# Kernel tuning notes

Measured on AMD Instinct MI355X. Metric: run time of the kernel, lower is better.

## Reference

```python
import jax, jax.numpy as jnp
import numpy as np

N = 50000   # nodes (subjects in population graph)
E = 800000  # edges (similarity graph, avg degree 16)
F = 128     # node features


def setup_inputs() -> dict:
    key = jax.random.key(0)
    ks = jax.random.split(key, 8)

    def glorot(k, shape):
        scale = 1.0 / np.sqrt(shape[0])
        return jax.random.normal(k, shape, jnp.float32) * scale

    x = jax.random.normal(ks[0], (N, F), jnp.float32)
    edge_index = jax.random.randint(ks[1], (2, E), 0, N, dtype=jnp.int64)
    return {
        "x": x,
        "edge_index": edge_index,
        "W1": glorot(ks[2], (F, 128)),   "b1": jnp.zeros((128,), jnp.float32),
        "W2": glorot(ks[3], (128, 64)),  "b2": jnp.zeros((64,), jnp.float32),
        "Wf1": glorot(ks[4], (64, 32)),  "bf1": jnp.zeros((32,), jnp.float32),
        "Wf2": glorot(ks[5], (32, 1)),   "bf2": jnp.zeros((1,), jnp.float32),
    }


def reference(x, edge_index, W1, b1, W2, b2, Wf1, bf1, Wf2, bf2):
    n = x.shape[0]
    # GCNConv (PyG default): add self-loops, symmetric deg^{-1/2} normalization
    loops = jnp.arange(n, dtype=edge_index.dtype)
    src = jnp.concatenate([edge_index[0], loops])  # [E+N]
    dst = jnp.concatenate([edge_index[1], loops])  # [E+N]
    deg = jax.ops.segment_sum(jnp.ones_like(dst, x.dtype), dst, num_segments=n)
    dinv = deg ** -0.5  # deg >= 1 thanks to self-loops
    norm = (dinv[src] * dinv[dst])[:, None]  # [E+N, 1]

    def gcn_conv(h, W, b):
        h = h @ W                                    # transform [n, out]
        msg = h[src] * norm                          # gather + normalize
        agg = jax.ops.segment_sum(msg, dst, num_segments=n)  # scatter-add
        return agg + b

    h = jnp.tanh(gcn_conv(x, W1, b1))
    h = jnp.tanh(gcn_conv(h, W2, b2))
    h = jnp.tanh(h @ Wf1 + bf1)
    return h @ Wf2 + bf2  # [n, 1] brain-age prediction
```

## Files before the change

kernel.cpp:

```cpp
#include <hip/hip_runtime.h>
#include <hip/hip_fp16.h>
#include <math.h>

#define TPB 256
#define CAP 64
#define BSHIFT 7
#define BSPAN 128
#define NBLK 256

__global__ __launch_bounds__(TPB) void detect_dtype(const int* __restrict__ e,
                                                    int* __restrict__ flag) {
  __shared__ int found;
  if (threadIdx.x == 0) found = 0;
  __syncthreads();
  int nz = 0;
  for (int i = threadIdx.x; i < 2048; i += TPB)
    nz |= (e[2 * i + 1] != 0) ? 1 : 0;
  if (nz) atomicOr(&found, 1);
  __syncthreads();
  if (threadIdx.x == 0) *flag = found;
}

__device__ __forceinline__ void load_edge(const void* eptr, int flag, int E,
                                          int e, int& s, int& d) {
  if (flag) {
    const int* p = (const int*)eptr;
    s = p[e];
    d = p[E + e];
  } else {
    const long long* p = (const long long*)eptr;
    s = (int)p[e];
    d = (int)p[E + e];
  }
}

__global__ __launch_bounds__(TPB) void bucket_count(const void* __restrict__ eptr,
                                                    const int* __restrict__ flag,
                                                    int* __restrict__ cnt,
                                                    int E, int nbuck, int chunk) {
  extern __shared__ int hist[];
  const int tid = threadIdx.x;
  const int fl = *flag;
  for (int b = tid; b < nbuck; b += TPB) hist[b] = 0;
  __syncthreads();
  const int start = blockIdx.x * chunk;
  const int end = min(E, start + chunk);
  for (int e = start + tid; e < end; e += TPB) {
    int s, d;
    load_edge(eptr, fl, E, e, s, d);
    atomicAdd(&hist[d >> BSHIFT], 1);
  }
  __syncthreads();
  for (int b = tid; b < nbuck; b += TPB)
    cnt[blockIdx.x * nbuck + b] = hist[b];
}

__global__ __launch_bounds__(TPB) void scan_col(int* __restrict__ cnt,
                                                int* __restrict__ colsum,
                                                int nbuck) {
  __shared__ int buf[TPB];
  const int b = blockIdx.x;
  const int tid = threadIdx.x;
  int v = cnt[tid * nbuck + b];
  buf[tid] = v;
  __syncthreads();
  for (int off = 1; off < TPB; off <<= 1) {
    int t = (tid >= off) ? buf[tid - off] : 0;
    __syncthreads();
    buf[tid] += t;
    __syncthreads();
  }
  cnt[tid * nbuck + b] = buf[tid] - v;
  if (tid == TPB - 1) colsum[b] = buf[tid];
}

__global__ __launch_bounds__(TPB) void scan_bstart(const int* __restrict__ colsum,
                                                   int* __restrict__ bstart,
                                                   int nbuck, int E) {
  __shared__ int buf[TPB];
  __shared__ int carry;
  const int tid = threadIdx.x;
  if (tid == 0) carry = 0;
  __syncthreads();
  for (int base = 0; base < nbuck; base += TPB) {
    int i = base + tid;
    int v = (i < nbuck) ? colsum[i] : 0;
    buf[tid] = v;
    __syncthreads();
    for (int off = 1; off < TPB; off <<= 1) {
      int t = (tid >= off) ? buf[tid - off] : 0;
      __syncthreads();
      buf[tid] += t;
      __syncthreads();
    }
    if (i < nbuck) bstart[i] = carry + buf[tid] - v;
    __syncthreads();
    if (tid == TPB - 1) carry += buf[tid];
    __syncthreads();
  }
  if (tid == 0) bstart[nbuck] = E;
}

__global__ __launch_bounds__(TPB) void bucket_scatter(const void* __restrict__ eptr,
                                                      const int* __restrict__ flag,
                                                      const int* __restrict__ cnt,
                                                      const int* __restrict__ bstart,
                                                      unsigned long long* __restrict__ pairs,
                                                      int E, int nbuck, int chunk) {
  extern __shared__ int cur[];
  const int tid = threadIdx.x;
  const int fl = *flag;
  for (int b = tid; b < nbuck; b += TPB)
    cur[b] = bstart[b] + cnt[blockIdx.x * nbuck + b];
  __syncthreads();
  const int start = blockIdx.x * chunk;
  const int end = min(E, start + chunk);
  for (int e = start + tid; e < end; e += TPB) {
    int s, d;
    load_edge(eptr, fl, E, e, s, d);
    int slot = atomicAdd(&cur[d >> BSHIFT], 1);
    pairs[slot] = ((unsigned long long)(unsigned)d << 32) | (unsigned)s;
  }
}

__global__ __launch_bounds__(TPB) void ell_build(const unsigned long long* __restrict__ pairs,
                                                 const int* __restrict__ bstart,
                                                 int* __restrict__ ell,
                                                 int* __restrict__ degi,
                                                 float* __restrict__ dinv,
                                                 int n) {
  __shared__ int cnt[BSPAN];
  const int b = blockIdx.x;
  const int tid = threadIdx.x;
  const int base = b << BSHIFT;
  for (int j = tid; j < BSPAN; j += TPB) cnt[j] = 0;
  __syncthreads();
  const int start = bstart[b];
  const int end = bstart[b + 1];
  for (int i = start + tid; i < end; i += TPB) {
    unsigned long long pr = pairs[i];
    int d = (int)(pr >> 32);
    int s = (int)(unsigned)pr;
    int slot = atomicAdd(&cnt[d - base], 1);
    if (slot < CAP) ell[(size_t)d * CAP + slot] = s;
  }
  __syncthreads();
  for (int j = tid; j < BSPAN; j += TPB) {
    int node = base + j;
    if (node < n) {
      int c = cnt[j];
      degi[node] = c;
      dinv[node] = rsqrtf((float)(c + 1));
    }
  }
}

template <int NC>
__global__ __launch_bounds__(TPB, 4) void gemm_fast(const float* __restrict__ A,
                                                    const float* __restrict__ W,
                                                    const float* __restrict__ dinv,
                                                    __half* __restrict__ out, int nrows) {
  constexpr int K = 128, TM = 64, BK = 32;
  constexpr int CPT = NC / 16;
  constexpr int AST = TM + 4;
  __shared__ float As[BK * AST];
  __shared__ float Ws[BK * NC];

  const int tid = threadIdx.x;
  const int tx = tid % 16;
  const int ty = tid / 16;
  const int r0 = ty * 4;
  const int block_row = blockIdx.x * TM;

  float acc[4][CPT];
#pragma unroll
  for (int r = 0; r < 4; r++)
#pragma unroll
    for (int c = 0; c < CPT; c++) acc[r][c] = 0.f;

  for (int k0 = 0; k0 < K; k0 += BK) {
#pragma unroll
    for (int i = 0; i < 2; i++) {
      int lid = tid + i * TPB;
      int r = lid / 8;
      int kk = (lid % 8) * 4;
      int gr = block_row + r;
      float4 v = make_float4(0.f, 0.f, 0.f, 0.f);
      if (gr < nrows) v = *(const float4*)&A[(size_t)gr * K + k0 + kk];
      As[(kk + 0) * AST + r] = v.x;
      As[(kk + 1) * AST + r] = v.y;
      As[(kk + 2) * AST + r] = v.z;
      As[(kk + 3) * AST + r] = v.w;
    }
#pragma unroll
    for (int i = 0; i < (BK * NC) / (4 * TPB); i++) {
      int lid = tid + i * TPB;
      int k = lid / (NC / 4);
      int c = (lid % (NC / 4)) * 4;
      *(float4*)&Ws[k * NC + c] = *(const float4*)&W[(size_t)(k0 + k) * NC + c];
    }
    __syncthreads();

#pragma unroll
    for (int k = 0; k < BK; k++) {
      float4 a = *(const float4*)&As[k * AST + r0];
      float av[4] = {a.x, a.y, a.z, a.w};
      float4 w0 = *(const float4*)&Ws[k * NC + tx * 4];
      float wv[CPT];
      wv[0] = w0.x; wv[1] = w0.y; wv[2] = w0.z; wv[3] = w0.w;
      if (NC == 128) {
        float4 w1 = *(const float4*)&Ws[k * NC + 64 + tx * 4];
        wv[4] = w1.x; wv[5] = w1.y; wv[6] = w1.z; wv[7] = w1.w;
      }
#pragma unroll
      for (int r = 0; r < 4; r++)
#pragma unroll
        for (int c = 0; c < CPT; c++) acc[r][c] += av[r] * wv[c];
    }
    __syncthreads();
  }

  union H4 { __half2 h[2]; uint2 u; };
#pragma unroll
  for (int r = 0; r < 4; r++) {
    int gr = block_row + r0 + r;
    if (gr >= nrows) continue;
    float di = dinv[gr];
    H4 p;
    p.h[0] = __float22half2_rn(make_float2(acc[r][0] * di, acc[r][1] * di));
    p.h[1] = __float22half2_rn(make_float2(acc[r][2] * di, acc[r][3] * di));
    *(uint2*)&out[(size_t)gr * NC + tx * 4] = p.u;
    if (NC == 128) {
      H4 q;
      q.h[0] = __float22half2_rn(make_float2(acc[r][4] * di, acc[r][5] * di));
      q.h[1] = __float22half2_rn(make_float2(acc[r][6] * di, acc[r][7] * di));
      *(uint2*)&out[(size_t)gr * NC + 64 + tx * 4] = q.u;
    }
  }
}

template <int NC>
__global__ __launch_bounds__(TPB) void gcn_aggregate(const int* __restrict__ degi,
                                                     const int* __restrict__ ell,
                                                     const __half* __restrict__ t,
                                                     const float* __restrict__ dinv,
                                                     const float* __restrict__ bias,
                                                     float* __restrict__ h, int n) {
  constexpr int LPN = 16;
  constexpr int CPL = NC / LPN;
  constexpr int NPB = TPB / LPN;
  int tid = threadIdx.x;
  int node = blockIdx.x * NPB + tid / LPN;
  int lane = tid % LPN;
  if (node >= n) return;

  int deg = degi[node];
  if (deg > CAP) deg = CAP;
  const int* nbr = &ell[(size_t)node * CAP];
  const __half* tp = t + (size_t)lane * CPL;

  float acc[CPL];
#pragma unroll
  for (int c = 0; c < CPL; c++) acc[c] = 0.f;

  union Ld { uint4 u4; uint2 u2; __half2 h[4]; };
  for (int j = 0; j < deg; j++) {
    int s = nbr[j];
    Ld v;
    if (CPL == 8) v.u4 = *(const uint4*)&tp[(size_t)s * NC];
    else          v.u2 = *(const uint2*)&tp[(size_t)s * NC];
#pragma unroll
    for (int c = 0; c < CPL / 2; c++) {
      float2 f = __half22float2(v.h[c]);
      acc[2 * c] += f.x;
      acc[2 * c + 1] += f.y;
    }
  }
  {
    Ld v;
    if (CPL == 8) v.u4 = *(const uint4*)&tp[(size_t)node * NC];
    else          v.u2 = *(const uint2*)&tp[(size_t)node * NC];
#pragma unroll
    for (int c = 0; c < CPL / 2; c++) {
      float2 f = __half22float2(v.h[c]);
      acc[2 * c] += f.x;
      acc[2 * c + 1] += f.y;
    }
  }

  float di = dinv[node];
  float* hp = &h[(size_t)node * NC + lane * CPL];
  const float* bp = &bias[lane * CPL];
#pragma unroll
  for (int c = 0; c < CPL; c += 4) {
    float4 b = *(const float4*)&bp[c];
    float4 r;
    r.x = tanhf(acc[c + 0] * di + b.x);
    r.y = tanhf(acc[c + 1] * di + b.y);
    r.z = tanhf(acc[c + 2] * di + b.z);
    r.w = tanhf(acc[c + 3] * di + b.w);
    *(float4*)&hp[c] = r;
  }
}

__global__ __launch_bounds__(TPB) void mlp_head(const float* __restrict__ h2,
                                                const float* __restrict__ Wf1,
                                                const float* __restrict__ bf1,
                                                const float* __restrict__ Wf2,
                                                const float* __restrict__ bf2,
                                                float* __restrict__ out, int n) {
  int row = blockIdx.x * TPB + threadIdx.x;
  if (row >= n) return;
  float acc[32];
#pragma unroll
  for (int j = 0; j < 32; j++) acc[j] = bf1[j];
#pragma unroll 4
  for (int k = 0; k < 64; k += 4) {
    float4 h4 = *(const float4*)&h2[(size_t)row * 64 + k];
    float hv[4] = {h4.x, h4.y, h4.z, h4.w};
#pragma unroll
    for (int kk = 0; kk < 4; kk++)
#pragma unroll
      for (int j = 0; j < 32; j++) acc[j] += hv[kk] * Wf1[(k + kk) * 32 + j];
  }
  float o = bf2[0];
#pragma unroll
  for (int j = 0; j < 32; j++) o += tanhf(acc[j]) * Wf2[j];
  out[row] = o;
}

extern "C" void kernel_launch(void* const* d_in, const int* in_sizes, int n_in,
                              void* d_out, int out_size, void* d_ws, size_t ws_size,
                              hipStream_t stream) {
  const float* x   = (const float*)d_in[0];
  const void*  eix = d_in[1];
  const float* W1  = (const float*)d_in[2];
  const float* b1  = (const float*)d_in[3];
  const float* W2  = (const float*)d_in[4];
  const float* b2  = (const float*)d_in[5];
  const float* Wf1 = (const float*)d_in[6];
  const float* bf1 = (const float*)d_in[7];
  const float* Wf2 = (const float*)d_in[8];
  const float* bf2 = (const float*)d_in[9];
  float* out = (float*)d_out;

  const int N = in_sizes[0] / 128;
  const int E = in_sizes[1] / 2;
  const int nb = (N + TPB - 1) / TPB;
  const int nbuck = (N + BSPAN - 1) >> BSHIFT;
  const int chunk = (E + NBLK - 1) / NBLK;
  const size_t histBytes = (size_t)nbuck * 4;

  char* ws = (char*)d_ws;
  size_t off = 0;
  int* degi = (int*)(ws + off); off += (size_t)N * 4;
  float* dinv = (float*)(ws + off); off += (size_t)N * 4;
  int* flag = (int*)(ws + off); off += 64;
  int* cnt = (int*)(ws + off); off += (size_t)NBLK * nbuck * 4;
  int* colsum = (int*)(ws + off); off += (size_t)(nbuck + 4) * 4;
  int* bstart = (int*)(ws + off); off += (size_t)(nbuck + 4) * 4;
  off = (off + 15) & ~(size_t)15;
  unsigned long long* pairs = (unsigned long long*)(ws + off); off += (size_t)E * 8;
  int* ell = (int*)(ws + off); off += (size_t)N * CAP * 4;
  off = (off + 15) & ~(size_t)15;
  __half* t1 = (__half*)(ws + off); off += (size_t)N * 128 * 2;
  float* h1 = (float*)(ws + off); off += (size_t)N * 128 * 4;
  float* h2 = (float*)(ws + off); off += (size_t)N * 64 * 4;
  __half* t2 = t1;
  (void)ws_size; (void)n_in; (void)out_size;

  detect_dtype<<<1, TPB, 0, stream>>>((const int*)eix, flag);
  bucket_count<<<NBLK, TPB, histBytes, stream>>>(eix, flag, cnt, E, nbuck, chunk);
  scan_col<<<nbuck, TPB, 0, stream>>>(cnt, colsum, nbuck);
  scan_bstart<<<1, TPB, 0, stream>>>(colsum, bstart, nbuck, E);
  bucket_scatter<<<NBLK, TPB, histBytes, stream>>>(eix, flag, cnt, bstart, pairs, E, nbuck, chunk);
  ell_build<<<nbuck, TPB, 0, stream>>>(pairs, bstart, ell, degi, dinv, N);

  gemm_fast<128><<<(N + 63) / 64, TPB, 0, stream>>>(x, W1, dinv, t1, N);
  gcn_aggregate<128><<<(N + 15) / 16, TPB, 0, stream>>>(degi, ell, t1, dinv, b1, h1, N);

  gemm_fast<64><<<(N + 63) / 64, TPB, 0, stream>>>(h1, W2, dinv, t2, N);
  gcn_aggregate<64><<<(N + 15) / 16, TPB, 0, stream>>>(degi, ell, t2, dinv, b2, h2, N);

  mlp_head<<<nb, TPB, 0, stream>>>(h2, Wf1, bf1, Wf2, bf2, out, N);
}
```

Before: 260.4 us.

## Fuse MLP head into layer-2 aggregation, store h1 as fp16, unroll gathers

Fuses the MLP head into the second GCN aggregation kernel using shared-memory rows and Wf1 staged in LDS, so the h2 buffer is neither written nor re-read. The layer-1 activations h1 are stored in fp16, with the second GEMM templated to read half inputs, which halves that traffic. The aggregation loops load neighbor indices as vectors and issue 4 or 8 feature gathers at a time to raise memory-level parallelism. Nontemporal hints are added on the pairs and ELL streams. The risks are reduced precision for h1 and extra shared memory plus a block barrier in the fused kernel.

```diff
diff --git a/kernel.cpp b/kernel.cpp
--- a/kernel.cpp
+++ b/kernel.cpp
@@ -7,6 +7,10 @@
 #define BSHIFT 7
 #define BSPAN 128
 #define NBLK 256
+
+typedef int   nt_i4 __attribute__((ext_vector_type(4)));
+typedef unsigned nt_u4 __attribute__((ext_vector_type(4)));
+typedef unsigned nt_u2 __attribute__((ext_vector_type(2)));
 
 __global__ __launch_bounds__(TPB) void detect_dtype(const int* __restrict__ e,
                                                     int* __restrict__ flag) {
@@ -119,7 +123,8 @@
     int s, d;
     load_edge(eptr, fl, E, e, s, d);
     int slot = atomicAdd(&cur[d >> BSHIFT], 1);
-    pairs[slot] = ((unsigned long long)(unsigned)d << 32) | (unsigned)s;
+    unsigned long long pv = ((unsigned long long)(unsigned)d << 32) | (unsigned)s;
+    __builtin_nontemporal_store(pv, &pairs[slot]);
   }
 }
 
@@ -138,11 +143,11 @@
   const int start = bstart[b];
   const int end = bstart[b + 1];
   for (int i = start + tid; i < end; i += TPB) {
-    unsigned long long pr = pairs[i];
+    unsigned long long pr = __builtin_nontemporal_load(&pairs[i]);
     int d = (int)(pr >> 32);
     int s = (int)(unsigned)pr;
     int slot = atomicAdd(&cnt[d - base], 1);
-    if (slot < CAP) ell[(size_t)d * CAP + slot] = s;
+    if (slot < CAP) __builtin_nontemporal_store(s, &ell[(size_t)d * CAP + slot]);
   }
   __syncthreads();
   for (int j = tid; j < BSPAN; j += TPB) {
@@ -155,8 +160,8 @@
   }
 }
 
-template <int NC>
-__global__ __launch_bounds__(TPB, 4) void gemm_fast(const float* __restrict__ A,
+template <int NC, typename AT>
+__global__ __launch_bounds__(TPB, 4) void gemm_fast(const AT* __restrict__ A,
                                                     const float* __restrict__ W,
                                                     const float* __restrict__ dinv,
                                                     __half* __restrict__ out, int nrows) {
@@ -186,7 +191,17 @@
       int kk = (lid % 8) * 4;
       int gr = block_row + r;
       float4 v = make_float4(0.f, 0.f, 0.f, 0.f);
-      if (gr < nrows) v = *(const float4*)&A[(size_t)gr * K + k0 + kk];
+      if (gr < nrows) {
+        if (sizeof(AT) == 4) {
+          v = *(const float4*)&A[(size_t)gr * K + k0 + kk];
+        } else {
+          uint2 raw = *(const uint2*)&A[(size_t)gr * K + k0 + kk];
+          const __half2* hh = (const __half2*)&raw;
+          float2 f0 = __half22float2(hh[0]);
+          float2 f1 = __half22float2(hh[1]);
+          v = make_float4(f0.x, f0.y, f1.x, f1.y);
+        }
+      }
       As[(kk + 0) * AST + r] = v.x;
       As[(kk + 1) * AST + r] = v.y;
       As[(kk + 2) * AST + r] = v.z;
@@ -239,16 +254,13 @@
   }
 }
 
-template <int NC>
-__global__ __launch_bounds__(TPB) void gcn_aggregate(const int* __restrict__ degi,
-                                                     const int* __restrict__ ell,
-                                                     const __half* __restrict__ t,
-                                                     const float* __restrict__ dinv,
-                                                     const float* __restrict__ bias,
-                                                     float* __restrict__ h, int n) {
-  constexpr int LPN = 16;
-  constexpr int CPL = NC / LPN;
-  constexpr int NPB = TPB / LPN;
+__global__ __launch_bounds__(TPB) void gcn_aggregate128(const int* __restrict__ degi,
+                                                        const int* __restrict__ ell,
+                                                        const __half* __restrict__ t,
+                                                        const float* __restrict__ dinv,
+                                                        const float* __restrict__ bias,
+                                                        __half* __restrict__ h, int n) {
+  constexpr int NC = 128, LPN = 16, CPL = 8, NPB = TPB / LPN;
   int tid = threadIdx.x;
   int node = blockIdx.x * NPB + tid / LPN;
   int lane = tid % LPN;
@@ -263,70 +275,147 @@
 #pragma unroll
   for (int c = 0; c < CPL; c++) acc[c] = 0.f;
 
-  union Ld { uint4 u4; uint2 u2; __half2 h[4]; };
-  for (int j = 0; j < deg; j++) {
-    int s = nbr[j];
-    Ld v;
-    if (CPL == 8) v.u4 = *(const uint4*)&tp[(size_t)s * NC];
-    else          v.u2 = *(const uint2*)&tp[(size_t)s * NC];
-#pragma unroll
-    for (int c = 0; c < CPL / 2; c++) {
+  union Ld { uint4 u4; __half2 h[4]; };
+  auto addv = [&](const Ld& v) {
+#pragma unroll
+    for (int c = 0; c < 4; c++) {
       float2 f = __half22float2(v.h[c]);
       acc[2 * c] += f.x;
       acc[2 * c + 1] += f.y;
     }
+  };
+
+  int j = 0;
+  for (; j + 8 <= deg; j += 8) {
+    nt_i4 n0 = __builtin_nontemporal_load((const nt_i4*)&nbr[j]);
+    nt_i4 n1 = __builtin_nontemporal_load((const nt_i4*)&nbr[j + 4]);
+    Ld v0, v1, v2, v3, v4, v5, v6, v7;
+    v0.u4 = *(const uint4*)&tp[(size_t)n0.x * NC];
+    v1.u4 = *(const uint4*)&tp[(size_t)n0.y * NC];
+    v2.u4 = *(const uint4*)&tp[(size_t)n0.z * NC];
+    v3.u4 = *(const uint4*)&tp[(size_t)n0.w * NC];
+    v4.u4 = *(const uint4*)&tp[(size_t)n1.x * NC];
+    v5.u4 = *(const uint4*)&tp[(size_t)n1.y * NC];
+    v6.u4 = *(const uint4*)&tp[(size_t)n1.z * NC];
+    v7.u4 = *(const uint4*)&tp[(size_t)n1.w * NC];
+    addv(v0); addv(v1); addv(v2); addv(v3);
+    addv(v4); addv(v5); addv(v6); addv(v7);
+  }
+  for (; j + 4 <= deg; j += 4) {
+    nt_i4 n0 = __builtin_nontemporal_load((const nt_i4*)&nbr[j]);
+    Ld v0, v1, v2, v3;
+    v0.u4 = *(const uint4*)&tp[(size_t)n0.x * NC];
+    v1.u4 = *(const uint4*)&tp[(size_t)n0.y * NC];
+    v2.u4 = *(const uint4*)&tp[(size_t)n0.z * NC];
+    v3.u4 = *(const uint4*)&tp[(size_t)n0.w * NC];
+    addv(v0); addv(v1); addv(v2); addv(v3);
+  }
+  for (; j < deg; j++) {
+    Ld v;
+    v.u4 = *(const uint4*)&tp[(size_t)nbr[j] * NC];
+    addv(v);
   }
   {
     Ld v;
-    if (CPL == 8) v.u4 = *(const uint4*)&tp[(size_t)node * NC];
-    else          v.u2 = *(const uint2*)&tp[(size_t)node * NC];
-#pragma unroll
-    for (int c = 0; c < CPL / 2; c++) {
-      float2 f = __half22float2(v.h[c]);
-      acc[2 * c] += f.x;
-      acc[2 * c + 1] += f.y;
-    }
+    v.u4 = *(const uint4*)&tp[(size_t)node * NC];
+    addv(v);
   }
 
   float di = dinv[node];
-  float* hp = &h[(size_t)node * NC + lane * CPL];
   const float* bp = &bias[lane * CPL];
+  float bv[CPL];
 #pragma unroll
   for (int c = 0; c < CPL; c += 4) {
     float4 b = *(const float4*)&bp[c];
-    float4 r;
-    r.x = tanhf(acc[c + 0] * di + b.x);
-    r.y = tanhf(acc[c + 1] * di + b.y);
-    r.z = tanhf(acc[c + 2] * di + b.z);
-    r.w = tanhf(acc[c + 3] * di + b.w);
-    *(float4*)&hp[c] = r;
-  }
-}
-
-__global__ __launch_bounds__(TPB) void mlp_head(const float* __restrict__ h2,
-                                                const float* __restrict__ Wf1,
-                                                const float* __restrict__ bf1,
-                                                const float* __restrict__ Wf2,
-                                                const float* __restrict__ bf2,
-                                                float* __restrict__ out, int n) {
-  int row = blockIdx.x * TPB + threadIdx.x;
-  if (row >= n) return;
-  float acc[32];
-#pragma unroll
-  for (int j = 0; j < 32; j++) acc[j] = bf1[j];
-#pragma unroll 4
-  for (int k = 0; k < 64; k += 4) {
-    float4 h4 = *(const float4*)&h2[(size_t)row * 64 + k];
-    float hv[4] = {h4.x, h4.y, h4.z, h4.w};
-#pragma unroll
-    for (int kk = 0; kk < 4; kk++)
-#pragma unroll
-      for (int j = 0; j < 32; j++) acc[j] += hv[kk] * Wf1[(k + kk) * 32 + j];
-  }
-  float o = bf2[0];
-#pragma unroll
-  for (int j = 0; j < 32; j++) o += tanhf(acc[j]) * Wf2[j];
-  out[row] = o;
+    bv[c] = b.x; bv[c + 1] = b.y; bv[c + 2] = b.z; bv[c + 3] = b.w;
+  }
+  union { __half2 hh[4]; nt_u4 u; } o;
+#pragma unroll
+  for (int c = 0; c < CPL; c += 2)
+    o.hh[c / 2] = __float22half2_rn(make_float2(tanhf(acc[c] * di + bv[c]),
+                                                tanhf(acc[c + 1] * di + bv[c + 1])));
+  __builtin_nontemporal_store(o.u, (nt_u4*)&h[(size_t)node * NC + lane * CPL]);
+}
+
+__global__ __launch_bounds__(TPB) void gcn_aggregate_head(
+    const int* __restrict__ degi, const int* __restrict__ ell,
+    const __half* __restrict__ t, const float* __restrict__ dinv,
+    const float* __restrict__ b2, const float* __restrict__ Wf1,
+    const float* __restrict__ bf1, const float* __restrict__ Wf2,
+    const float* __restrict__ bf2, float* __restrict__ out, int n) {
+  constexpr int NC = 64, LPN = 16, NPB = TPB / LPN;
+  __shared__ float hrow[NPB][68];
+  __shared__ float Wf1s[64 * 32];
+  __shared__ float Wf2s[32];
+  const int tid = threadIdx.x;
+
+#pragma unroll
+  for (int i = 0; i < 2; i++) {
+    int lid = tid + i * TPB;
+    *(float4*)&Wf1s[lid * 4] = *(const float4*)&Wf1[lid * 4];
+  }
+  if (tid < 32) Wf2s[tid] = Wf2[tid];
+
+  const int g = tid / LPN;
+  const int ll = tid % LPN;
+  const int node = blockIdx.x * NPB + g;
+  const bool active = node < n;
+
+  float acc[4] = {0.f, 0.f, 0.f, 0.f};
+  if (active) {
+    int deg = degi[node];
+    if (deg > CAP) deg = CAP;
+    const int* nbr = &ell[(size_t)node * CAP];
+    const __half* tp = t + (size_t)ll * 4;
+    union Ld { uint2 u2; __half2 h[2]; };
+    auto addv = [&](const Ld& v) {
+      float2 f0 = __half22float2(v.h[0]);
+      float2 f1 = __half22float2(v.h[1]);
+      acc[0] += f0.x; acc[1] += f0.y; acc[2] += f1.x; acc[3] += f1.y;
+    };
+    int j = 0;
+    for (; j + 4 <= deg; j += 4) {
+      nt_i4 nn = __builtin_nontemporal_load((const nt_i4*)&nbr[j]);
+      Ld v0, v1, v2, v3;
+      v0.u2 = *(const uint2*)&tp[(size_t)nn.x * NC];
+      v1.u2 = *(const uint2*)&tp[(size_t)nn.y * NC];
+      v2.u2 = *(const uint2*)&tp[(size_t)nn.z * NC];
+      v3.u2 = *(const uint2*)&tp[(size_t)nn.w * NC];
+      addv(v0); addv(v1); addv(v2); addv(v3);
+    }
+    for (; j < deg; j++) {
+      Ld v;
+      v.u2 = *(const uint2*)&tp[(size_t)nbr[j] * NC];
+      addv(v);
+    }
+    {
+      Ld v;
+      v.u2 = *(const uint2*)&tp[(size_t)node * NC];
+      addv(v);
+    }
+    float di = dinv[node];
+    float4 b = *(const float4*)&b2[ll * 4];
+    hrow[g][ll * 4 + 0] = tanhf(acc[0] * di + b.x);
+    hrow[g][ll * 4 + 1] = tanhf(acc[1] * di + b.y);
+    hrow[g][ll * 4 + 2] = tanhf(acc[2] * di + b.z);
+    hrow[g][ll * 4 + 3] = tanhf(acc[3] * di + b.w);
+  }
+  __syncthreads();
+
+  float hid0 = bf1[ll];
+  float hid1 = bf1[ll + 16];
+#pragma unroll 8
+  for (int i = 0; i < 64; i++) {
+    float hv = hrow[g][i];
+    hid0 += hv * Wf1s[i * 32 + ll];
+    hid1 += hv * Wf1s[i * 32 + ll + 16];
+  }
+  float p = tanhf(hid0) * Wf2s[ll] + tanhf(hid1) * Wf2s[ll + 16];
+  p += __shfl_down(p, 8, 16);
+  p += __shfl_down(p, 4, 16);
+  p += __shfl_down(p, 2, 16);
+  p += __shfl_down(p, 1, 16);
+  if (active && ll == 0) out[node] = p + bf2[0];
 }
 
 extern "C" void kernel_launch(void* const* d_in, const int* in_sizes, int n_in,
@@ -346,7 +435,6 @@
 
   const int N = in_sizes[0] / 128;
   const int E = in_sizes[1] / 2;
-  const int nb = (N + TPB - 1) / TPB;
   const int nbuck = (N + BSPAN - 1) >> BSHIFT;
   const int chunk = (E + NBLK - 1) / NBLK;
   const size_t histBytes = (size_t)nbuck * 4;
@@ -364,8 +452,7 @@
   int* ell = (int*)(ws + off); off += (size_t)N * CAP * 4;
   off = (off + 15) & ~(size_t)15;
   __half* t1 = (__half*)(ws + off); off += (size_t)N * 128 * 2;
-  float* h1 = (float*)(ws + off); off += (size_t)N * 128 * 4;
-  float* h2 = (float*)(ws + off); off += (size_t)N * 64 * 4;
+  __half* h1 = (__half*)(ws + off); off += (size_t)N * 128 * 2;
   __half* t2 = t1;
   (void)ws_size; (void)n_in; (void)out_size;
 
@@ -376,11 +463,10 @@
   bucket_scatter<<<NBLK, TPB, histBytes, stream>>>(eix, flag, cnt, bstart, pairs, E, nbuck, chunk);
   ell_build<<<nbuck, TPB, 0, stream>>>(pairs, bstart, ell, degi, dinv, N);
 
-  gemm_fast<128><<<(N + 63) / 64, TPB, 0, stream>>>(x, W1, dinv, t1, N);
-  gcn_aggregate<128><<<(N + 15) / 16, TPB, 0, stream>>>(degi, ell, t1, dinv, b1, h1, N);
-
-  gemm_fast<64><<<(N + 63) / 64, TPB, 0, stream>>>(h1, W2, dinv, t2, N);
-  gcn_aggregate<64><<<(N + 15) / 16, TPB, 0, stream>>>(degi, ell, t2, dinv, b2, h2, N);
-
-  mlp_head<<<nb, TPB, 0, stream>>>(h2, Wf1, bf1, Wf2, bf2, out, N);
-}
+  gemm_fast<128, float><<<(N + 63) / 64, TPB, 0, stream>>>(x, W1, dinv, t1, N);
+  gcn_aggregate128<<<(N + 15) / 16, TPB, 0, stream>>>(degi, ell, t1, dinv, b1, h1, N);
+
+  gemm_fast<64, __half><<<(N + 63) / 64, TPB, 0, stream>>>(h1, W2, dinv, t2, N);
+  gcn_aggregate_head<<<(N + 15) / 16, TPB, 0, stream>>>(degi, ell, t2, dinv, b2,
+                                                        Wf1, bf1, Wf2, bf2, out, N);
+}
```

Measured after the change: 253.9 us. 1.03x faster.
